# Kernel optimization log

Measured on AMD Instinct MI355X. Metric: run time of the kernel, lower is better.

## Reference

```python
import jax, jax.numpy as jnp
import numpy as np

B, DZ, DE, M, H = 4096, 2048, 128, 32, 1024
GATE_TEMP = 1.0


def setup_inputs() -> dict:
    key = jax.random.key(0)
    ks = jax.random.split(key, 6)
    s = lambda k, shape, sc: jax.random.normal(k, shape, dtype=jnp.float32) * sc
    return dict(
        z=s(ks[0], (B, DZ), 1.0),
        base_W=s(ks[1], (3, DZ), 0.02),
        base_b=jnp.zeros((3,), jnp.float32),
        gate_W=s(ks[2], (DE, DZ), 0.02),
        gate_b=jnp.zeros((DE,), jnp.float32),
        E=s(ks[3], (M, DE), 0.02),              # material embedding table
        W1=s(ks[4], (M, H, DZ + DE), 0.02),     # stacked first-layer weights
        b1=jnp.zeros((M, H), jnp.float32),
        W2=s(ks[5], (M, 3, H), 0.02),           # stacked second-layer weights
        b2=jnp.zeros((M, 3), jnp.float32),
    )


def _l2norm(x, eps=1e-12):
    # matches F.normalize(dim=-1): x / max(||x||_2, eps)
    n = jnp.linalg.norm(x, axis=-1, keepdims=True)
    return x / jnp.maximum(n, eps)


def reference(z, base_W, base_b, gate_W, gate_b, E, W1, b1, W2, b2):
    dz = z.shape[1]
    # base head: [B, 3]
    b = z @ base_W.T + base_b
    # gate similarities (routing logits): [B, M]
    q = _l2norm(z @ gate_W.T + gate_b)
    sims = q @ _l2norm(E).T
    # Per-material 2-layer MLP on cat([z, E_m]) fused as grouped GEMMs.
    # Split W1 into the z-part and embedding-part of the concat input.
    W1z, W1e = W1[:, :, :dz], W1[:, :, dz:]
    emb_term = jnp.einsum('me,mhe->mh', E, W1e)        # [M, H], shared across batch
    h = jax.nn.gelu(
        jnp.einsum('bi,mhi->bmh', z, W1z) + emb_term[None] + b1[None],
        approximate=False,
    )                                                   # [B, M, H]
    delta = jnp.einsum('bmh,moh->bmo', h, W2) + b2[None]  # [B, M, 3]
    # scale_delta_by_gate=False path; dropout inactive at inference.
    L = (b[:, None, :] + delta).reshape(z.shape[0], -1)   # [B, 3*M]
    return L, sims
```

## Files before the change

### kernel.cpp

```cpp
#include <hip/hip_runtime.h>
#include <hip/hip_bf16.h>
#include <math.h>

#define B_ROWS 4096
#define DZ     2048
#define DE     128
#define M_EXP  32
#define H_DIM  1024
#define NBIG   32768
#define NEXTRA 256
#define NTOT   (NBIG + NEXTRA)
#define W1_LD  (DZ + DE)

typedef _Float16 half8 __attribute__((ext_vector_type(8)));
typedef float    f32x4 __attribute__((ext_vector_type(4)));

#define AS1 __attribute__((address_space(1)))
#define AS3 __attribute__((address_space(3)))

__device__ __forceinline__ void async_copy16(const void* g, void* l) {
  __builtin_amdgcn_global_load_lds((const AS1 void*)g, (AS3 void*)l, 16, 0, 0);
}

__device__ __forceinline__ half8 cvt8(const float4& a, const float4& b) {
  half8 h = {(_Float16)a.x, (_Float16)a.y, (_Float16)a.z, (_Float16)a.w,
             (_Float16)b.x, (_Float16)b.y, (_Float16)b.z, (_Float16)b.w};
  return h;
}

__device__ __forceinline__ float gelu_f(float x) {
  float u = fabsf(x) * 0.70710678118654752f;
  float t = 1.0f / fmaf(0.3275911f, u, 1.0f);
  float poly = t * fmaf(t, fmaf(t, fmaf(t, fmaf(t, 1.061405429f, -1.453152027f),
                                        1.421413741f), -0.284496736f), 0.254829592f);
  float er = 1.0f - poly * __expf(-u * u);
  er = copysignf(er, x);
  return 0.5f * x * (1.0f + er);
}

__global__ __launch_bounds__(256) void k_cvt_z(const float* __restrict__ z,
                                               _Float16* __restrict__ zh) {
  long i = ((long)blockIdx.x * 256 + threadIdx.x) * 8;
  float4 a = *(const float4*)(z + i);
  float4 b = *(const float4*)(z + i + 4);
  *(half8*)(zh + i) = cvt8(a, b);
}

__global__ __launch_bounds__(256) void k_cvt_w1(const float* __restrict__ W1,
                                                const float* __restrict__ E,
                                                const float* __restrict__ b1,
                                                _Float16* __restrict__ W1h,
                                                float* __restrict__ hbias) {
  const long n = blockIdx.x;
  const int  t = threadIdx.x;
  const float* src = W1 + n * W1_LD;
  float4 a = *(const float4*)(src + t * 8);
  float4 b = *(const float4*)(src + t * 8 + 4);
  *(half8*)(W1h + n * DZ + t * 8) = cvt8(a, b);
  if (t < 32) {
    int m = (int)(n >> 10);
    float4 w = *(const float4*)(src + DZ + t * 4);
    float4 e = *(const float4*)(E + m * DE + t * 4);
    float p = w.x * e.x + w.y * e.y + w.z * e.z + w.w * e.w;
    p += __shfl_xor(p, 16);
    p += __shfl_xor(p, 8);
    p += __shfl_xor(p, 4);
    p += __shfl_xor(p, 2);
    p += __shfl_xor(p, 1);
    if (t == 0) hbias[n] = p + b1[n];
  }
}

__global__ __launch_bounds__(256) void k_cvt_small(const float* __restrict__ gate_W,
                                                   const float* __restrict__ base_W,
                                                   _Float16* __restrict__ W1h) {
  int r = blockIdx.x;
  int t = threadIdx.x;
  const float* src = nullptr;
  if (r < 128)       src = gate_W + (long)r * DZ;
  else if (r < 131)  src = base_W + (long)(r - 128) * DZ;
  _Float16* dst = W1h + (long)(NBIG + r) * DZ + t * 8;
  if (src) {
    float4 a = *(const float4*)(src + t * 8);
    float4 b = *(const float4*)(src + t * 8 + 4);
    *(half8*)dst = cvt8(a, b);
  } else {
    half8 zv = {(_Float16)0, (_Float16)0, (_Float16)0, (_Float16)0,
                (_Float16)0, (_Float16)0, (_Float16)0, (_Float16)0};
    *(half8*)dst = zv;
  }
}

__global__ __launch_bounds__(256, 4) void k_gemm(const _Float16* __restrict__ A,
                                                 const _Float16* __restrict__ Bm,
                                                 const float* __restrict__ hbias,
                                                 const float* __restrict__ W2,
                                                 float* __restrict__ Lout,
                                                 float* __restrict__ qraw) {
  __shared__ _Float16 sm[8192];

  int flat = blockIdx.y * gridDim.x + blockIdx.x;
  int wg   = (flat & 7) * 1032 + (flat >> 3);
  const int tN = wg >> 5;
  const int tM = wg & 31;

  const int tid = threadIdx.x;
  const int w = tid >> 6, l = tid & 63;
  const int wm = w >> 1, wn = w & 1;
  const int rl = l & 15, lg = l >> 4;

  const int srow  = tid >> 2;
  const int sgoff = ((tid & 3) ^ ((srow >> 1) & 3)) * 8;
  const _Float16* gA = A  + (long)(tM * 128 + srow) * DZ + sgoff;
  const _Float16* gB = Bm + (long)(tN * 128 + srow) * DZ + sgoff;

#define STAGE(kt) do { \
    async_copy16(gA + (kt) * 32,           &sm[tid * 8]); \
    async_copy16(gA + 64 * DZ + (kt) * 32, &sm[2048 + tid * 8]); \
    async_copy16(gB + (kt) * 32,           &sm[4096 + tid * 8]); \
    async_copy16(gB + 64 * DZ + (kt) * 32, &sm[6144 + tid * 8]); } while (0)

  const int aswz  = (lg ^ ((rl >> 1) & 3)) * 8;
  const int offA0 = (wm * 64 + rl) * 32 + aswz;
  const int offB0 = 4096 + (wn * 64 + rl) * 32 + aswz;

  half8 af[4], bf[4];
  f32x4 acc[4][4];
  f32x4 z4 = {0.f, 0.f, 0.f, 0.f};
#pragma unroll
  for (int i = 0; i < 4; ++i)
#pragma unroll
    for (int j = 0; j < 4; ++j) acc[i][j] = z4;

  STAGE(0);

#pragma unroll 2
  for (int kt = 0; kt < 64; ++kt) {
    __syncthreads();
#pragma unroll
    for (int i = 0; i < 4; ++i) af[i] = *(const half8*)&sm[offA0 + i * 512];
#pragma unroll
    for (int j = 0; j < 4; ++j) bf[j] = *(const half8*)&sm[offB0 + j * 512];
    __builtin_amdgcn_s_setprio(1);
#pragma unroll
    for (int i = 0; i < 4; ++i)
#pragma unroll
      for (int j = 0; j < 4; ++j)
        acc[i][j] = __builtin_amdgcn_mfma_f32_16x16x32_f16(af[i], bf[j], acc[i][j], 0, 0, 0);
    __builtin_amdgcn_s_setprio(0);
    __syncthreads();
    if (kt < 63) STAGE(kt + 1);
  }

  if (tN < 256) {
    const int m = tN >> 3;
    float hb[4], w2v[3][4];
#pragma unroll
    for (int j = 0; j < 4; ++j) {
      int gcol = tN * 128 + wn * 64 + j * 16 + rl;
      int he   = gcol & (H_DIM - 1);
      hb[j] = hbias[gcol];
#pragma unroll
      for (int o = 0; o < 3; ++o) w2v[o][j] = W2[((long)m * 3 + o) * H_DIM + he];
    }
#pragma unroll
    for (int i = 0; i < 4; ++i) {
      const int growb = tM * 128 + wm * 64 + i * 16 + lg * 4;
#pragma unroll
      for (int r = 0; r < 4; ++r) {
        int grow = growb + r;
        float hv[4];
#pragma unroll
        for (int j = 0; j < 4; ++j) hv[j] = gelu_f(acc[i][j][r] + hb[j]);
#pragma unroll
        for (int o = 0; o < 3; ++o) {
          float p = hv[0] * w2v[o][0] + hv[1] * w2v[o][1] + hv[2] * w2v[o][2] + hv[3] * w2v[o][3];
          p += __shfl_xor(p, 1);
          p += __shfl_xor(p, 2);
          p += __shfl_xor(p, 4);
          p += __shfl_xor(p, 8);
          if (rl == o) atomicAdd(&Lout[(long)grow * 96 + m * 3 + o], p);
        }
      }
    }
  } else {
#pragma unroll
    for (int i = 0; i < 4; ++i) {
      const int growb = tM * 128 + wm * 64 + i * 16 + lg * 4;
#pragma unroll
      for (int r = 0; r < 4; ++r) {
        int grow = growb + r;
        int c0 = (tN - 256) * 128 + wn * 64 + rl;
#pragma unroll
        for (int j = 0; j < 4; ++j)
          qraw[(long)grow * 256 + c0 + j * 16] = acc[i][j][r];
      }
    }
  }
}

__global__ __launch_bounds__(128) void k_post(const float* __restrict__ qraw,
                                              const float* __restrict__ gate_b,
                                              const float* __restrict__ base_b,
                                              const float* __restrict__ E,
                                              const float* __restrict__ b2,
                                              float* __restrict__ out) {
  const int b = blockIdx.x;
  const int t = threadIdx.x;
  __shared__ float qs[DE];
  __shared__ float invE[M_EXP];
  __shared__ float wsum[2];
  __shared__ float pA[M_EXP], pB[M_EXP];

  if (t < 32) {
    float ss = 0.f;
    const float* er = E + t * DE;
    for (int e = 0; e < DE; ++e) { float v = er[e]; ss += v * v; }
    invE[t] = 1.0f / fmaxf(sqrtf(ss), 1e-12f);
  }

  float val = qraw[(long)b * 256 + t] + gate_b[t];
  float ss = val * val;
  ss += __shfl_xor(ss, 1);  ss += __shfl_xor(ss, 2);  ss += __shfl_xor(ss, 4);
  ss += __shfl_xor(ss, 8);  ss += __shfl_xor(ss, 16); ss += __shfl_xor(ss, 32);
  if ((t & 63) == 0) wsum[t >> 6] = ss;
  __syncthreads();
  float inv = 1.0f / fmaxf(sqrtf(wsum[0] + wsum[1]), 1e-12f);
  qs[t] = val * inv;
  __syncthreads();

  {
    int m = t & 31, hf = t >> 5;
    const float* er = E + m * DE + hf * 32;
    const float* qq = qs + hf * 32;
    float p = 0.f;
#pragma unroll
    for (int e = 0; e < 32; ++e) p += qq[e] * er[e];
    p += __shfl_xor(p, 32);
    if (t < 32) pA[m] = p;
    else if (t >= 64 && t < 96) pB[m] = p;
    __syncthreads();
    if (t < 32) out[(long)B_ROWS * 96 + (long)b * 32 + t] = (pA[t] + pB[t]) * invE[t];
  }

  if (t < 96) {
    int o = t % 3;
    float bv = qraw[(long)b * 256 + 128 + o] + base_b[o];
    out[(long)b * 96 + t] += bv + b2[t];
  }
}

extern "C" void kernel_launch(void* const* d_in, const int* in_sizes, int n_in,
                              void* d_out, int out_size, void* d_ws, size_t ws_size,
                              hipStream_t stream) {
  const float* z      = (const float*)d_in[0];
  const float* base_W = (const float*)d_in[1];
  const float* base_b = (const float*)d_in[2];
  const float* gate_W = (const float*)d_in[3];
  const float* gate_b = (const float*)d_in[4];
  const float* E      = (const float*)d_in[5];
  const float* W1     = (const float*)d_in[6];
  const float* b1     = (const float*)d_in[7];
  const float* W2     = (const float*)d_in[8];
  const float* b2     = (const float*)d_in[9];
  float* out = (float*)d_out;

  char* ws = (char*)d_ws;
  const size_t off_zh    = 0;
  const size_t off_w1h   = off_zh  + (size_t)B_ROWS * DZ * 2;
  const size_t off_hbias = off_w1h + (size_t)NTOT * DZ * 2;
  const size_t off_qraw  = off_hbias + (size_t)NBIG * 4;
  _Float16* zh    = (_Float16*)(ws + off_zh);
  _Float16* W1h   = (_Float16*)(ws + off_w1h);
  float*    hbias = (float*)(ws + off_hbias);
  float*    qraw  = (float*)(ws + off_qraw);

  hipMemsetAsync(d_out, 0, (size_t)B_ROWS * 96 * sizeof(float), stream);

  k_cvt_z<<<(B_ROWS * DZ) / (256 * 8), 256, 0, stream>>>(z, zh);
  k_cvt_w1<<<NBIG, 256, 0, stream>>>(W1, E, b1, W1h, hbias);
  k_cvt_small<<<NEXTRA, 256, 0, stream>>>(gate_W, base_W, W1h);
  k_gemm<<<dim3(258, 32), 256, 0, stream>>>(zh, W1h, hbias, W2, out, qraw);
  k_post<<<B_ROWS, 128, 0, stream>>>(qraw, gate_b, base_b, E, b2, out);
}
```

Measured before the change: 915.8 us.

## Widen GEMM tile to 128x256 with triple-buffered LDS software pipeline

The main fp16 GEMM tile grows from 128x128 to 128x256 per block, so each wave accumulates a 4x8 grid of MFMA fragments, halving B re-reads of A and the number of blocks. The LDS becomes a three-stage ring with split A/B half loads, explicit vmcnt waits and raw barriers, so global loads overlap MFMA work across two phases per k-step. Occupancy drops to 2 blocks per CU and register pressure rises from the doubled accumulators. The epilogue is widened to match (8 column fragments, new expert and qraw indexing).

```diff
diff --git a/kernel.cpp b/kernel.cpp
--- a/kernel.cpp
+++ b/kernel.cpp
@@ -91,16 +91,16 @@
   }
 }
 
-__global__ __launch_bounds__(256, 4) void k_gemm(const _Float16* __restrict__ A,
+__global__ __launch_bounds__(256, 2) void k_gemm(const _Float16* __restrict__ A,
                                                  const _Float16* __restrict__ Bm,
                                                  const float* __restrict__ hbias,
                                                  const float* __restrict__ W2,
                                                  float* __restrict__ Lout,
                                                  float* __restrict__ qraw) {
-  __shared__ _Float16 sm[8192];
+  __shared__ _Float16 sm[3][12288];
 
   int flat = blockIdx.y * gridDim.x + blockIdx.x;
-  int wg   = (flat & 7) * 1032 + (flat >> 3);
+  int wg   = (flat & 7) * 516 + (flat >> 3);
   const int tN = wg >> 5;
   const int tM = wg & 31;
 
@@ -112,52 +112,92 @@
   const int srow  = tid >> 2;
   const int sgoff = ((tid & 3) ^ ((srow >> 1) & 3)) * 8;
   const _Float16* gA = A  + (long)(tM * 128 + srow) * DZ + sgoff;
-  const _Float16* gB = Bm + (long)(tN * 128 + srow) * DZ + sgoff;
-
-#define STAGE(kt) do { \
-    async_copy16(gA + (kt) * 32,           &sm[tid * 8]); \
-    async_copy16(gA + 64 * DZ + (kt) * 32, &sm[2048 + tid * 8]); \
-    async_copy16(gB + (kt) * 32,           &sm[4096 + tid * 8]); \
-    async_copy16(gB + 64 * DZ + (kt) * 32, &sm[6144 + tid * 8]); } while (0)
+  const _Float16* gB = Bm + (long)(tN * 256 + srow) * DZ + sgoff;
+
+#define STAGE_A(sb, kt) do { \
+    async_copy16(gA + (kt) * 32,            &sm[sb][tid * 8]); \
+    async_copy16(gA + 64 * DZ + (kt) * 32,  &sm[sb][2048 + tid * 8]); } while (0)
+#define STAGE_B0(sb, kt) do { \
+    async_copy16(gB + (kt) * 32,            &sm[sb][4096 + tid * 8]); \
+    async_copy16(gB + 64 * DZ + (kt) * 32,  &sm[sb][6144 + tid * 8]); } while (0)
+#define STAGE_B1(sb, kt) do { \
+    async_copy16(gB + 128 * DZ + (kt) * 32, &sm[sb][8192 + tid * 8]); \
+    async_copy16(gB + 192 * DZ + (kt) * 32, &sm[sb][10240 + tid * 8]); } while (0)
 
   const int aswz  = (lg ^ ((rl >> 1) & 3)) * 8;
   const int offA0 = (wm * 64 + rl) * 32 + aswz;
-  const int offB0 = 4096 + (wn * 64 + rl) * 32 + aswz;
-
-  half8 af[4], bf[4];
-  f32x4 acc[4][4];
+  const int offB0 = 4096 + (wn * 128 + rl) * 32 + aswz;
+
+  half8 afE[4], afO[4], bf03[4], bf47[4];
+  f32x4 acc[4][8];
   f32x4 z4 = {0.f, 0.f, 0.f, 0.f};
 #pragma unroll
   for (int i = 0; i < 4; ++i)
 #pragma unroll
-    for (int j = 0; j < 4; ++j) acc[i][j] = z4;
-
-  STAGE(0);
-
-#pragma unroll 2
-  for (int kt = 0; kt < 64; ++kt) {
-    __syncthreads();
-#pragma unroll
-    for (int i = 0; i < 4; ++i) af[i] = *(const half8*)&sm[offA0 + i * 512];
-#pragma unroll
-    for (int j = 0; j < 4; ++j) bf[j] = *(const half8*)&sm[offB0 + j * 512];
-    __builtin_amdgcn_s_setprio(1);
-#pragma unroll
-    for (int i = 0; i < 4; ++i)
-#pragma unroll
-      for (int j = 0; j < 4; ++j)
-        acc[i][j] = __builtin_amdgcn_mfma_f32_16x16x32_f16(af[i], bf[j], acc[i][j], 0, 0, 0);
-    __builtin_amdgcn_s_setprio(0);
-    __syncthreads();
-    if (kt < 63) STAGE(kt + 1);
-  }
-
-  if (tN < 256) {
-    const int m = tN >> 3;
-    float hb[4], w2v[3][4];
-#pragma unroll
-    for (int j = 0; j < 4; ++j) {
-      int gcol = tN * 128 + wn * 64 + j * 16 + rl;
+    for (int j = 0; j < 8; ++j) acc[i][j] = z4;
+
+#define RD_AF(dst, sl) do { _Pragma("unroll") for (int _i = 0; _i < 4; ++_i) \
+    dst[_i] = *(const half8*)&sm[sl][offA0 + _i * 512]; } while (0)
+#define RD_B03(sl) do { _Pragma("unroll") for (int _j = 0; _j < 4; ++_j) \
+    bf03[_j] = *(const half8*)&sm[sl][offB0 + _j * 512]; } while (0)
+#define RD_B47(sl) do { _Pragma("unroll") for (int _j = 0; _j < 4; ++_j) \
+    bf47[_j] = *(const half8*)&sm[sl][offB0 + (4 + _j) * 512]; } while (0)
+
+#define MFMA_J03(af_) do { __builtin_amdgcn_s_setprio(1); \
+    _Pragma("unroll") for (int _i = 0; _i < 4; ++_i) \
+    _Pragma("unroll") for (int _j = 0; _j < 4; ++_j) \
+      acc[_i][_j] = __builtin_amdgcn_mfma_f32_16x16x32_f16(af_[_i], bf03[_j], acc[_i][_j], 0, 0, 0); \
+    __builtin_amdgcn_s_setprio(0); } while (0)
+#define MFMA_J47(af_) do { __builtin_amdgcn_s_setprio(1); \
+    _Pragma("unroll") for (int _i = 0; _i < 4; ++_i) \
+    _Pragma("unroll") for (int _j = 0; _j < 4; ++_j) \
+      acc[_i][4 + _j] = __builtin_amdgcn_mfma_f32_16x16x32_f16(af_[_i], bf47[_j], acc[_i][4 + _j], 0, 0, 0); \
+    __builtin_amdgcn_s_setprio(0); } while (0)
+
+#define BAR() do { asm volatile("" ::: "memory"); __builtin_amdgcn_s_barrier(); asm volatile("" ::: "memory"); } while (0)
+#define SBAR0 __builtin_amdgcn_sched_barrier(0)
+#define VM6 asm volatile("s_waitcnt vmcnt(6)" ::: "memory")
+#define VM0 asm volatile("s_waitcnt vmcnt(0)" ::: "memory")
+
+#define PH_A(sl, sb, kt, AFc) do { \
+    STAGE_A(sb, kt); STAGE_B0(sb, kt); BAR(); \
+    RD_B47(sl); SBAR0; MFMA_J03(AFc); } while (0)
+#define PH_A_N(sl, AFc) do { BAR(); \
+    RD_B47(sl); SBAR0; MFMA_J03(AFc); } while (0)
+#define PH_B(slN, sb, kt, AFc, AFn, CERT) do { \
+    STAGE_B1(sb, kt); CERT; BAR(); \
+    RD_AF(AFn, slN); RD_B03(slN); SBAR0; MFMA_J47(AFc); } while (0)
+#define PH_B_N(slN, AFc, AFn, CERT) do { CERT; BAR(); \
+    RD_AF(AFn, slN); RD_B03(slN); SBAR0; MFMA_J47(AFc); } while (0)
+#define PH_B_LAST(AFc) do { BAR(); SBAR0; MFMA_J47(AFc); } while (0)
+
+  STAGE_A(0, 0); STAGE_B0(0, 0); STAGE_B1(0, 0);
+  STAGE_A(1, 1); STAGE_B0(1, 1); STAGE_B1(1, 1);
+  VM6;
+  BAR();
+  RD_AF(afE, 0); RD_B03(0);
+
+#pragma unroll 1
+  for (int n = 0; n < 10; ++n) {
+    const int t6 = 6 * n;
+    PH_A(0, 2, t6 + 2, afE); PH_B(1, 2, t6 + 2, afE, afO, VM6);
+    PH_A(1, 0, t6 + 3, afO); PH_B(2, 0, t6 + 3, afO, afE, VM6);
+    PH_A(2, 1, t6 + 4, afE); PH_B(0, 1, t6 + 4, afE, afO, VM6);
+    PH_A(0, 2, t6 + 5, afO); PH_B(1, 2, t6 + 5, afO, afE, VM6);
+    PH_A(1, 0, t6 + 6, afE); PH_B(2, 0, t6 + 6, afE, afO, VM6);
+    PH_A(2, 1, t6 + 7, afO); PH_B(0, 1, t6 + 7, afO, afE, VM6);
+  }
+  PH_A(0, 2, 62, afE); PH_B(1, 2, 62, afE, afO, VM6);
+  PH_A(1, 0, 63, afO); PH_B(2, 0, 63, afO, afE, VM6);
+  PH_A_N(2, afE);      PH_B_N(0, afE, afO, VM0);
+  PH_A_N(0, afO);      PH_B_LAST(afO);
+
+  if (tN < 128) {
+    const int m = tN >> 2;
+    float hb[8], w2v[3][8];
+#pragma unroll
+    for (int j = 0; j < 8; ++j) {
+      int gcol = tN * 256 + wn * 128 + j * 16 + rl;
       int he   = gcol & (H_DIM - 1);
       hb[j] = hbias[gcol];
 #pragma unroll
@@ -169,12 +209,14 @@
 #pragma unroll
       for (int r = 0; r < 4; ++r) {
         int grow = growb + r;
-        float hv[4];
-#pragma unroll
-        for (int j = 0; j < 4; ++j) hv[j] = gelu_f(acc[i][j][r] + hb[j]);
+        float hv[8];
+#pragma unroll
+        for (int j = 0; j < 8; ++j) hv[j] = gelu_f(acc[i][j][r] + hb[j]);
 #pragma unroll
         for (int o = 0; o < 3; ++o) {
-          float p = hv[0] * w2v[o][0] + hv[1] * w2v[o][1] + hv[2] * w2v[o][2] + hv[3] * w2v[o][3];
+          float p = 0.f;
+#pragma unroll
+          for (int j = 0; j < 8; ++j) p = fmaf(hv[j], w2v[o][j], p);
           p += __shfl_xor(p, 1);
           p += __shfl_xor(p, 2);
           p += __shfl_xor(p, 4);
@@ -190,9 +232,9 @@
 #pragma unroll
       for (int r = 0; r < 4; ++r) {
         int grow = growb + r;
-        int c0 = (tN - 256) * 128 + wn * 64 + rl;
-#pragma unroll
-        for (int j = 0; j < 4; ++j)
+        int c0 = wn * 128 + rl;
+#pragma unroll
+        for (int j = 0; j < 8; ++j)
           qraw[(long)grow * 256 + c0 + j * 16] = acc[i][j][r];
       }
     }
@@ -280,6 +322,6 @@
   k_cvt_z<<<(B_ROWS * DZ) / (256 * 8), 256, 0, stream>>>(z, zh);
   k_cvt_w1<<<NBIG, 256, 0, stream>>>(W1, E, b1, W1h, hbias);
   k_cvt_small<<<NEXTRA, 256, 0, stream>>>(gate_W, base_W, W1h);
-  k_gemm<<<dim3(258, 32), 256, 0, stream>>>(zh, W1h, hbias, W2, out, qraw);
+  k_gemm<<<dim3(129, 32), 256, 0, stream>>>(zh, W1h, hbias, W2, out, qraw);
   k_post<<<B_ROWS, 128, 0, stream>>>(qraw, gate_b, base_b, E, b2, out);
 }
```

New measurement: 784.5 us. 14.3% less time.
